# Optimization experiments

Hardware: AMD Instinct MI355X
Metric: run time of the kernel (lower is better)

The kernel has to match this reference:

```python
import jax, jax.numpy as jnp
import numpy as np

ALPHA = 0.2  # LeakyReLU negative slope
MASK_VAL = -9e15


def setup_inputs() -> dict:
    key = jax.random.key(0)
    k1, k2, k3, k4 = jax.random.split(key, 4)
    N, F_IN, F_OUT = 8192, 512, 64
    x = jax.random.normal(k1, (N, F_IN), dtype=jnp.float32)
    adj = jax.random.randint(k2, (N, N), 0, 2, dtype=jnp.int32)
    W = jax.random.normal(k3, (F_IN, F_OUT), dtype=jnp.float32) * (1.414 / np.sqrt(F_IN))
    a = jax.random.normal(k4, (2 * F_OUT, 1), dtype=jnp.float32) * 0.1
    return {"x": x, "adj": adj, "W": W, "a": a}


def reference(x, adj, W, a):
    # h = x @ W : [N, F_OUT]
    h = x @ W
    F_OUT = h.shape[1]
    # additive attention decomposed: score_ij = leaky_relu(a1.h_i + a2.h_j)
    # (mathematically identical to cat([h_i, h_j]) @ a, without the N^2*2F tensor)
    a1 = a[:F_OUT, 0]
    a2 = a[F_OUT:, 0]
    f1 = h @ a1  # [N]
    f2 = h @ a2  # [N]
    e = jax.nn.leaky_relu(f1[:, None] + f2[None, :], negative_slope=ALPHA)  # [N, N]
    e = jnp.where(adj > 0, e, MASK_VAL)
    attention = jax.nn.softmax(e, axis=1)  # dropout p=0.0 / eval mode -> identity
    h_prime = attention @ h  # [N, F_OUT]
    return jax.nn.elu(h_prime)  # concat=True path
```

## Files before the change

kernel.cpp:

```cpp
#include <hip/hip_runtime.h>
#include <stdint.h>

#define NN 8192
#define FIN 512
#define FOUT 64
#define ALPHA 0.2f
#define TJ 512
#define NT (NN / TJ)

typedef float f32x4 __attribute__((ext_vector_type(4)));
typedef int   i32x4 __attribute__((ext_vector_type(4)));
typedef short bf16x8 __attribute__((ext_vector_type(8)));

__device__ __forceinline__ unsigned short f2bf(float f) {
  union { float f; unsigned u; } v; v.f = f;
  unsigned r = (v.u + 0x7fffu + ((v.u >> 16) & 1u)) >> 16;
  return (unsigned short)r;
}

__global__ __launch_bounds__(256) void prep_kernel(
    const float* __restrict__ x, const float* __restrict__ W,
    const float* __restrict__ a, unsigned short* __restrict__ bpack,
    float* __restrict__ f1, float* __restrict__ f2) {
  const int lane = threadIdx.x & 63;
  const int g = blockIdx.x * 4 + (threadIdx.x >> 6);
  const int i0 = g * 8;

  float acc[8];
#pragma unroll
  for (int r = 0; r < 8; ++r) acc[r] = 0.0f;

  for (int k = 0; k < FIN; k += 4) {
    float w0 = W[(k + 0) * FOUT + lane];
    float w1 = W[(k + 1) * FOUT + lane];
    float w2 = W[(k + 2) * FOUT + lane];
    float w3 = W[(k + 3) * FOUT + lane];
#pragma unroll
    for (int r = 0; r < 8; ++r) {
      f32x4 xv = *(const f32x4*)(x + (size_t)(i0 + r) * FIN + k);
      acc[r] = fmaf(xv[0], w0, acc[r]);
      acc[r] = fmaf(xv[1], w1, acc[r]);
      acc[r] = fmaf(xv[2], w2, acc[r]);
      acc[r] = fmaf(xv[3], w3, acc[r]);
    }
  }

  const float a1c = a[lane];
  const float a2c = a[FOUT + lane];
#pragma unroll
  for (int r = 0; r < 8; ++r) {
    float p1 = acc[r] * a1c;
    float p2 = acc[r] * a2c;
#pragma unroll
    for (int off = 32; off >= 1; off >>= 1) {
      p1 += __shfl_xor(p1, off, 64);
      p2 += __shfl_xor(p2, off, 64);
    }
    if (lane == 0) { f1[i0 + r] = p1; f2[i0 + r] = p2; }
  }

  unsigned short hs[8];
#pragma unroll
  for (int r = 0; r < 8; ++r) hs[r] = f2bf(acc[r]);
  const int jb = i0 >> 5;
  const int kg = (i0 >> 3) & 3;
  const int cb = lane >> 4;
  const int rr = lane & 15;
  *(uint4*)(bpack + ((size_t)jb * 2048 + cb * 512 + kg * 128 + rr * 8)) = *(uint4*)hs;
}

__global__ __launch_bounds__(1024, 8) void attn_kernel(
    const int* __restrict__ adj, const unsigned short* __restrict__ bpack,
    const float* __restrict__ f1, const float* __restrict__ f2,
    float* __restrict__ out) {
  __shared__ __align__(16) char lds[16 * 16 * 64 * 4];
  __shared__ float lds_den[16];

  char* pwb0 = lds;
  char* pwb1 = lds + 16384;
  float (*lds_num)[16][64] = (float (*)[16][64])lds;

  const int tid = threadIdx.x;
  const int lane = tid & 63;
  const int wv = tid >> 6;
  const int rg = blockIdx.x;
  const int r15 = lane & 15;
  const int kgrp = lane >> 4;

  const int row_w = rg * 16 + wv;
  const float f1w = f1[row_w];
  const int* adjw = adj + (size_t)row_w * NN;

  int ard = r15 * 1024 + wv * 64 + kgrp * 16;
  ard ^= (r15 & 7) << 4;
  int awr = wv * 1024 + lane * 8;
  awr ^= (wv & 7) << 4;

  f32x4 acc0 = {0.f, 0.f, 0.f, 0.f};
  f32x4 acc1 = acc0, acc2 = acc0, acc3 = acc0;
  float den = 0.0f;

  i32x4 a0 = *(const i32x4*)(adjw + lane * 4);
  i32x4 a1 = *(const i32x4*)(adjw + 256 + lane * 4);

  for (int t = 0; t < NT; ++t) {
    const int j0 = t * TJ;
    f32x4 fA = *(const f32x4*)(f2 + j0 + lane * 4);
    f32x4 fB = *(const f32x4*)(f2 + j0 + 256 + lane * 4);

    unsigned short ws[8];
    float dsum = 0.0f;
#pragma unroll
    for (int e = 0; e < 4; ++e) {
      float s = f1w + fA[e];
      float l = fmaxf(s, ALPHA * s);
      float ev = __expf(l);
      float wv_ = (a0[e] > 0) ? ev : 0.0f;
      dsum += wv_;
      ws[e] = f2bf(wv_);
    }
#pragma unroll
    for (int e = 0; e < 4; ++e) {
      float s = f1w + fB[e];
      float l = fmaxf(s, ALPHA * s);
      float ev = __expf(l);
      float wv_ = (a1[e] > 0) ? ev : 0.0f;
      dsum += wv_;
      ws[4 + e] = f2bf(wv_);
    }
    den += dsum;

    char* pwb = (t & 1) ? pwb1 : pwb0;
    *(uint2*)(pwb + awr) = *(uint2*)&ws[0];
    *(uint2*)(pwb + awr + 512) = *(uint2*)&ws[4];

    __syncthreads();

    const int jn = ((t + 1) & (NT - 1)) * TJ;
    a0 = *(const i32x4*)(adjw + jn + lane * 4);
    a1 = *(const i32x4*)(adjw + jn + 256 + lane * 4);

    bf16x8 afrag = *(bf16x8*)(pwb + ard);
    const unsigned short* bp = bpack + ((size_t)(t * 16 + wv) * 2048 + lane * 8);
    bf16x8 b0 = *(const bf16x8*)(bp);
    bf16x8 b1 = *(const bf16x8*)(bp + 512);
    bf16x8 b2 = *(const bf16x8*)(bp + 1024);
    bf16x8 b3 = *(const bf16x8*)(bp + 1536);

    acc0 = __builtin_amdgcn_mfma_f32_16x16x32_bf16(afrag, b0, acc0, 0, 0, 0);
    acc1 = __builtin_amdgcn_mfma_f32_16x16x32_bf16(afrag, b1, acc1, 0, 0, 0);
    acc2 = __builtin_amdgcn_mfma_f32_16x16x32_bf16(afrag, b2, acc2, 0, 0, 0);
    acc3 = __builtin_amdgcn_mfma_f32_16x16x32_bf16(afrag, b3, acc3, 0, 0, 0);
  }

#pragma unroll
  for (int off = 1; off <= 32; off <<= 1) den += __shfl_xor(den, off, 64);

  __syncthreads();

#pragma unroll
  for (int r = 0; r < 4; ++r) {
    lds_num[wv][kgrp * 4 + r][0 * 16 + r15] = acc0[r];
    lds_num[wv][kgrp * 4 + r][1 * 16 + r15] = acc1[r];
    lds_num[wv][kgrp * 4 + r][2 * 16 + r15] = acc2[r];
    lds_num[wv][kgrp * 4 + r][3 * 16 + r15] = acc3[r];
  }
  if (lane == 0) lds_den[wv] = den;
  __syncthreads();

  {
    const int orow = tid >> 6;
    const int ocol = tid & 63;
    float s = 0.0f;
#pragma unroll
    for (int v = 0; v < 16; ++v) s += lds_num[v][orow][ocol];
    float vv = s / lds_den[orow];
    out[(size_t)(rg * 16 + orow) * FOUT + ocol] = (vv > 0.0f) ? vv : (__expf(vv) - 1.0f);
  }
}

extern "C" void kernel_launch(void* const* d_in, const int* in_sizes, int n_in,
                              void* d_out, int out_size, void* d_ws, size_t ws_size,
                              hipStream_t stream) {
  const float* x = (const float*)d_in[0];
  const int* adj = (const int*)d_in[1];
  const float* W = (const float*)d_in[2];
  const float* a = (const float*)d_in[3];
  float* out = (float*)d_out;

  char* ws = (char*)d_ws;
  unsigned short* bpack = (unsigned short*)ws;
  float* f1 = (float*)(ws + (size_t)FOUT * NN * 2);
  float* f2 = f1 + NN;

  hipLaunchKernelGGL(prep_kernel, dim3(256), dim3(256), 0, stream, x, W, a, bpack, f1, f2);
  hipLaunchKernelGGL(attn_kernel, dim3(512), dim3(1024), 0, stream, adj, bpack, f1, f2, out);
}
```

Before: 127.7 us.

## Pack adjacency into bitmask in a separate pass and prefetch bits in attention

Adds a compact kernel that streams the int32 adjacency matrix once with wide, highly parallel loads and writes a 1-bit-per-entry mask. The attention kernel then reads 8 MB of bits instead of 256 MB of int32 inside its MFMA loop, and software-prefetches the next tile's bits and f2 values. Each lane now handles 8 contiguous columns with a single 16-byte LDS store, and the occupancy hint in the launch bounds is lowered. The extra launch still reads all of adj, so any gain depends on the compaction pass streaming closer to peak bandwidth than the latency-bound attention loop did.

```diff
diff --git a/kernel.cpp b/kernel.cpp
--- a/kernel.cpp
+++ b/kernel.cpp
@@ -16,6 +16,37 @@
   union { float f; unsigned u; } v; v.f = f;
   unsigned r = (v.u + 0x7fffu + ((v.u >> 16) & 1u)) >> 16;
   return (unsigned short)r;
+}
+
+__device__ __forceinline__ unsigned packbits(i32x4 a, i32x4 b) {
+  unsigned r = 0;
+#pragma unroll
+  for (int e = 0; e < 4; ++e) r |= (a[e] > 0 ? 1u : 0u) << e;
+#pragma unroll
+  for (int e = 0; e < 4; ++e) r |= (b[e] > 0 ? 1u : 0u) << (4 + e);
+  return r;
+}
+
+__global__ __launch_bounds__(256) void compact_kernel(
+    const int* __restrict__ adj, unsigned char* __restrict__ bits) {
+  const int lane = threadIdx.x & 63;
+  const int wid = blockIdx.x * 4 + (threadIdx.x >> 6);
+  const int* p0 = adj + (size_t)wid * 2048 + lane * 8;
+
+  i32x4 va0 = *(const i32x4*)(p0);
+  i32x4 vb0 = *(const i32x4*)(p0 + 4);
+  i32x4 va1 = *(const i32x4*)(p0 + 512);
+  i32x4 vb1 = *(const i32x4*)(p0 + 516);
+  i32x4 va2 = *(const i32x4*)(p0 + 1024);
+  i32x4 vb2 = *(const i32x4*)(p0 + 1028);
+  i32x4 va3 = *(const i32x4*)(p0 + 1536);
+  i32x4 vb3 = *(const i32x4*)(p0 + 1540);
+
+  unsigned char* ob = bits + (size_t)wid * 256 + lane;
+  ob[0]   = (unsigned char)packbits(va0, vb0);
+  ob[64]  = (unsigned char)packbits(va1, vb1);
+  ob[128] = (unsigned char)packbits(va2, vb2);
+  ob[192] = (unsigned char)packbits(va3, vb3);
 }
 
 __global__ __launch_bounds__(256) void prep_kernel(
@@ -69,8 +100,8 @@
   *(uint4*)(bpack + ((size_t)jb * 2048 + cb * 512 + kg * 128 + rr * 8)) = *(uint4*)hs;
 }
 
-__global__ __launch_bounds__(1024, 8) void attn_kernel(
-    const int* __restrict__ adj, const unsigned short* __restrict__ bpack,
+__global__ __launch_bounds__(1024, 4) void attn_kernel(
+    const unsigned char* __restrict__ bits, const unsigned short* __restrict__ bpack,
     const float* __restrict__ f1, const float* __restrict__ f2,
     float* __restrict__ out) {
   __shared__ __align__(16) char lds[16 * 16 * 64 * 4];
@@ -89,68 +120,67 @@
 
   const int row_w = rg * 16 + wv;
   const float f1w = f1[row_w];
-  const int* adjw = adj + (size_t)row_w * NN;
+  const unsigned char* bitsrow = bits + (size_t)row_w * (NN / 8);
 
   int ard = r15 * 1024 + wv * 64 + kgrp * 16;
   ard ^= (r15 & 7) << 4;
-  int awr = wv * 1024 + lane * 8;
+  int awr = wv * 1024 + lane * 16;
   awr ^= (wv & 7) << 4;
 
   f32x4 acc0 = {0.f, 0.f, 0.f, 0.f};
   f32x4 acc1 = acc0, acc2 = acc0, acc3 = acc0;
   float den = 0.0f;
 
-  i32x4 a0 = *(const i32x4*)(adjw + lane * 4);
-  i32x4 a1 = *(const i32x4*)(adjw + 256 + lane * 4);
+  unsigned bcur = bitsrow[lane];
+  f32x4 fA = *(const f32x4*)(f2 + lane * 8);
+  f32x4 fB = *(const f32x4*)(f2 + lane * 8 + 4);
 
   for (int t = 0; t < NT; ++t) {
-    const int j0 = t * TJ;
-    f32x4 fA = *(const f32x4*)(f2 + j0 + lane * 4);
-    f32x4 fB = *(const f32x4*)(f2 + j0 + 256 + lane * 4);
-
-    unsigned short ws[8];
-    float dsum = 0.0f;
-#pragma unroll
-    for (int e = 0; e < 4; ++e) {
-      float s = f1w + fA[e];
-      float l = fmaxf(s, ALPHA * s);
-      float ev = __expf(l);
-      float wv_ = (a0[e] > 0) ? ev : 0.0f;
-      dsum += wv_;
-      ws[e] = f2bf(wv_);
-    }
-#pragma unroll
-    for (int e = 0; e < 4; ++e) {
-      float s = f1w + fB[e];
-      float l = fmaxf(s, ALPHA * s);
-      float ev = __expf(l);
-      float wv_ = (a1[e] > 0) ? ev : 0.0f;
-      dsum += wv_;
-      ws[4 + e] = f2bf(wv_);
-    }
-    den += dsum;
-
-    char* pwb = (t & 1) ? pwb1 : pwb0;
-    *(uint2*)(pwb + awr) = *(uint2*)&ws[0];
-    *(uint2*)(pwb + awr + 512) = *(uint2*)&ws[4];
-
-    __syncthreads();
-
-    const int jn = ((t + 1) & (NT - 1)) * TJ;
-    a0 = *(const i32x4*)(adjw + jn + lane * 4);
-    a1 = *(const i32x4*)(adjw + jn + 256 + lane * 4);
-
-    bf16x8 afrag = *(bf16x8*)(pwb + ard);
     const unsigned short* bp = bpack + ((size_t)(t * 16 + wv) * 2048 + lane * 8);
     bf16x8 b0 = *(const bf16x8*)(bp);
     bf16x8 b1 = *(const bf16x8*)(bp + 512);
     bf16x8 b2 = *(const bf16x8*)(bp + 1024);
     bf16x8 b3 = *(const bf16x8*)(bp + 1536);
 
+    const int tn = (t + 1) & (NT - 1);
+    unsigned bnxt = bitsrow[tn * 64 + lane];
+    f32x4 nfA = *(const f32x4*)(f2 + tn * TJ + lane * 8);
+    f32x4 nfB = *(const f32x4*)(f2 + tn * TJ + lane * 8 + 4);
+
+    unsigned short ws8[8];
+    float dsum = 0.0f;
+#pragma unroll
+    for (int e = 0; e < 4; ++e) {
+      float s = f1w + fA[e];
+      float l = fmaxf(s, ALPHA * s);
+      float ev = __expf(l);
+      float w_ = ((bcur >> e) & 1u) ? ev : 0.0f;
+      dsum += w_;
+      ws8[e] = f2bf(w_);
+    }
+#pragma unroll
+    for (int e = 0; e < 4; ++e) {
+      float s = f1w + fB[e];
+      float l = fmaxf(s, ALPHA * s);
+      float ev = __expf(l);
+      float w_ = ((bcur >> (4 + e)) & 1u) ? ev : 0.0f;
+      dsum += w_;
+      ws8[4 + e] = f2bf(w_);
+    }
+    den += dsum;
+
+    char* pwb = (t & 1) ? pwb1 : pwb0;
+    *(uint4*)(pwb + awr) = *(uint4*)ws8;
+
+    __syncthreads();
+
+    bf16x8 afrag = *(bf16x8*)(pwb + ard);
     acc0 = __builtin_amdgcn_mfma_f32_16x16x32_bf16(afrag, b0, acc0, 0, 0, 0);
     acc1 = __builtin_amdgcn_mfma_f32_16x16x32_bf16(afrag, b1, acc1, 0, 0, 0);
     acc2 = __builtin_amdgcn_mfma_f32_16x16x32_bf16(afrag, b2, acc2, 0, 0, 0);
     acc3 = __builtin_amdgcn_mfma_f32_16x16x32_bf16(afrag, b3, acc3, 0, 0, 0);
+
+    bcur = bnxt; fA = nfA; fB = nfB;
   }
 
 #pragma unroll
@@ -192,7 +222,9 @@
   unsigned short* bpack = (unsigned short*)ws;
   float* f1 = (float*)(ws + (size_t)FOUT * NN * 2);
   float* f2 = f1 + NN;
-
+  unsigned char* bits = (unsigned char*)(ws + (2u << 20));
+
+  hipLaunchKernelGGL(compact_kernel, dim3(8192), dim3(256), 0, stream, adj, bits);
   hipLaunchKernelGGL(prep_kernel, dim3(256), dim3(256), 0, stream, x, W, a, bpack, f1, f2);
-  hipLaunchKernelGGL(attn_kernel, dim3(512), dim3(1024), 0, stream, adj, bpack, f1, f2, out);
-}
+  hipLaunchKernelGGL(attn_kernel, dim3(512), dim3(1024), 0, stream, bits, bpack, f1, f2, out);
+}
```

Result: no change. 127.0 us (-0.5%).

## Process 32 rows per block to reuse bpack fragments across two MFMA tiles

Applied to the files above, without the earlier changes.

Each block now handles 32 output rows instead of 16, so every wave computes attention weights for two rows and reuses each loaded h fragment for two MFMA tiles. This halves bpack global reads per output row and halves the grid. The adjacency prefetch is now two tiles deep and the barrier is hand-written asm. The final cross-wave reduction is restructured into two phases with vectorised output stores. In exchange, register pressure and LDS use grow (64 KB per block), which may reduce occupancy.

```diff
diff --git a/kernel.cpp b/kernel.cpp
--- a/kernel.cpp
+++ b/kernel.cpp
@@ -7,8 +7,10 @@
 #define ALPHA 0.2f
 #define TJ 512
 #define NT (NN / TJ)
+#define RB 32
 
 typedef float f32x4 __attribute__((ext_vector_type(4)));
+typedef float f32x2 __attribute__((ext_vector_type(2)));
 typedef int   i32x4 __attribute__((ext_vector_type(4)));
 typedef short bf16x8 __attribute__((ext_vector_type(8)));
 
@@ -69,16 +71,11 @@
   *(uint4*)(bpack + ((size_t)jb * 2048 + cb * 512 + kg * 128 + rr * 8)) = *(uint4*)hs;
 }
 
-__global__ __launch_bounds__(1024, 8) void attn_kernel(
+__global__ __launch_bounds__(1024) void fused_kernel(
     const int* __restrict__ adj, const unsigned short* __restrict__ bpack,
     const float* __restrict__ f1, const float* __restrict__ f2,
     float* __restrict__ out) {
-  __shared__ __align__(16) char lds[16 * 16 * 64 * 4];
-  __shared__ float lds_den[16];
-
-  char* pwb0 = lds;
-  char* pwb1 = lds + 16384;
-  float (*lds_num)[16][64] = (float (*)[16][64])lds;
+  __shared__ __align__(16) char lds[65536 + 128];
 
   const int tid = threadIdx.x;
   const int lane = tid & 63;
@@ -87,95 +84,159 @@
   const int r15 = lane & 15;
   const int kgrp = lane >> 4;
 
-  const int row_w = rg * 16 + wv;
-  const float f1w = f1[row_w];
-  const int* adjw = adj + (size_t)row_w * NN;
-
-  int ard = r15 * 1024 + wv * 64 + kgrp * 16;
-  ard ^= (r15 & 7) << 4;
-  int awr = wv * 1024 + lane * 8;
-  awr ^= (wv & 7) << 4;
-
-  f32x4 acc0 = {0.f, 0.f, 0.f, 0.f};
-  f32x4 acc1 = acc0, acc2 = acc0, acc3 = acc0;
-  float den = 0.0f;
-
-  i32x4 a0 = *(const i32x4*)(adjw + lane * 4);
-  i32x4 a1 = *(const i32x4*)(adjw + 256 + lane * 4);
-
-  for (int t = 0; t < NT; ++t) {
-    const int j0 = t * TJ;
-    f32x4 fA = *(const f32x4*)(f2 + j0 + lane * 4);
-    f32x4 fB = *(const f32x4*)(f2 + j0 + 256 + lane * 4);
-
-    unsigned short ws[8];
-    float dsum = 0.0f;
-#pragma unroll
-    for (int e = 0; e < 4; ++e) {
-      float s = f1w + fA[e];
-      float l = fmaxf(s, ALPHA * s);
-      float ev = __expf(l);
-      float wv_ = (a0[e] > 0) ? ev : 0.0f;
-      dsum += wv_;
-      ws[e] = f2bf(wv_);
-    }
-#pragma unroll
-    for (int e = 0; e < 4; ++e) {
-      float s = f1w + fB[e];
-      float l = fmaxf(s, ALPHA * s);
-      float ev = __expf(l);
-      float wv_ = (a1[e] > 0) ? ev : 0.0f;
-      dsum += wv_;
-      ws[4 + e] = f2bf(wv_);
-    }
-    den += dsum;
-
-    char* pwb = (t & 1) ? pwb1 : pwb0;
-    *(uint2*)(pwb + awr) = *(uint2*)&ws[0];
-    *(uint2*)(pwb + awr + 512) = *(uint2*)&ws[4];
-
-    __syncthreads();
-
-    const int jn = ((t + 1) & (NT - 1)) * TJ;
-    a0 = *(const i32x4*)(adjw + jn + lane * 4);
-    a1 = *(const i32x4*)(adjw + jn + 256 + lane * 4);
-
-    bf16x8 afrag = *(bf16x8*)(pwb + ard);
-    const unsigned short* bp = bpack + ((size_t)(t * 16 + wv) * 2048 + lane * 8);
-    bf16x8 b0 = *(const bf16x8*)(bp);
-    bf16x8 b1 = *(const bf16x8*)(bp + 512);
-    bf16x8 b2 = *(const bf16x8*)(bp + 1024);
-    bf16x8 b3 = *(const bf16x8*)(bp + 1536);
-
-    acc0 = __builtin_amdgcn_mfma_f32_16x16x32_bf16(afrag, b0, acc0, 0, 0, 0);
-    acc1 = __builtin_amdgcn_mfma_f32_16x16x32_bf16(afrag, b1, acc1, 0, 0, 0);
-    acc2 = __builtin_amdgcn_mfma_f32_16x16x32_bf16(afrag, b2, acc2, 0, 0, 0);
-    acc3 = __builtin_amdgcn_mfma_f32_16x16x32_bf16(afrag, b3, acc3, 0, 0, 0);
-  }
-
-#pragma unroll
-  for (int off = 1; off <= 32; off <<= 1) den += __shfl_xor(den, off, 64);
-
-  __syncthreads();
-
-#pragma unroll
-  for (int r = 0; r < 4; ++r) {
-    lds_num[wv][kgrp * 4 + r][0 * 16 + r15] = acc0[r];
-    lds_num[wv][kgrp * 4 + r][1 * 16 + r15] = acc1[r];
-    lds_num[wv][kgrp * 4 + r][2 * 16 + r15] = acc2[r];
-    lds_num[wv][kgrp * 4 + r][3 * 16 + r15] = acc3[r];
-  }
-  if (lane == 0) lds_den[wv] = den;
-  __syncthreads();
+  const int row0 = rg * RB + wv;
+  const int row1 = row0 + 16;
+  const float f1v0 = f1[row0];
+  const float f1v1 = f1[row1];
+  const int* adj0 = adj + (size_t)row0 * NN;
+  const int* adj1 = adj + (size_t)row1 * NN;
+
+  const int aw0 = (wv * 1024 + lane * 16) ^ ((wv & 7) << 4);
+  const int aw1 = ((wv + 16) * 1024 + lane * 16) ^ ((wv & 7) << 4);
+  const int ar0 = (r15 * 1024 + wv * 64 + kgrp * 16) ^ ((r15 & 7) << 4);
+  const int ar1 = ((16 + r15) * 1024 + wv * 64 + kgrp * 16) ^ ((r15 & 7) << 4);
+
+  f32x4 acc00 = {0.f,0.f,0.f,0.f}, acc01 = acc00, acc02 = acc00, acc03 = acc00;
+  f32x4 acc10 = acc00, acc11 = acc00, acc12 = acc00, acc13 = acc00;
+  float den0 = 0.0f, den1 = 0.0f;
+
+  const int jl = lane * 8;
+
+  i32x4 sA0 = *(const i32x4*)(adj0 + jl);
+  i32x4 sA1 = *(const i32x4*)(adj0 + jl + 4);
+  i32x4 sB0 = *(const i32x4*)(adj1 + jl);
+  i32x4 sB1 = *(const i32x4*)(adj1 + jl + 4);
+  f32x4 sFA = *(const f32x4*)(f2 + jl);
+  f32x4 sFB = *(const f32x4*)(f2 + jl + 4);
+  i32x4 tA0 = *(const i32x4*)(adj0 + TJ + jl);
+  i32x4 tA1 = *(const i32x4*)(adj0 + TJ + jl + 4);
+  i32x4 tB0 = *(const i32x4*)(adj1 + TJ + jl);
+  i32x4 tB1 = *(const i32x4*)(adj1 + TJ + jl + 4);
+  f32x4 tFA = *(const f32x4*)(f2 + TJ + jl);
+  f32x4 tFB = *(const f32x4*)(f2 + TJ + jl + 4);
+
+#define FUSED_ITER(T_, CA0, CA1, CB0, CB1, CFA, CFB) do {                           \
+    const int t_ = (T_);                                                            \
+              \
+    const unsigned short* bp = bpack + ((size_t)(t_ * 16 + wv) * 2048) + lane * 8;  \
+    bf16x8 b0 = *(const bf16x8*)(bp);                                               \
+    bf16x8 b1 = *(const bf16x8*)(bp + 512);                                         \
+    bf16x8 b2 = *(const bf16x8*)(bp + 1024);                                        \
+    bf16x8 b3 = *(const bf16x8*)(bp + 1536);                                        \
+                              \
+    unsigned short w0[8], w1[8];                                                    \
+    _Pragma("unroll")                                                               \
+    for (int e = 0; e < 4; ++e) {                                                   \
+      float s0 = f1v0 + CFA[e];                                                     \
+      float v0 = (CA0[e] > 0) ? __expf(fmaxf(s0, ALPHA * s0)) : 0.0f;               \
+      den0 += v0; w0[e] = f2bf(v0);                                                 \
+      float s1 = f1v1 + CFA[e];                                                     \
+      float v1 = (CB0[e] > 0) ? __expf(fmaxf(s1, ALPHA * s1)) : 0.0f;               \
+      den1 += v1; w1[e] = f2bf(v1);                                                 \
+    }                                                                               \
+    _Pragma("unroll")                                                               \
+    for (int e = 0; e < 4; ++e) {                                                   \
+      float s0 = f1v0 + CFB[e];                                                     \
+      float v0 = (CA1[e] > 0) ? __expf(fmaxf(s0, ALPHA * s0)) : 0.0f;               \
+      den0 += v0; w0[4 + e] = f2bf(v0);                                             \
+      float s1 = f1v1 + CFB[e];                                                     \
+      float v1 = (CB1[e] > 0) ? __expf(fmaxf(s1, ALPHA * s1)) : 0.0f;               \
+      den1 += v1; w1[4 + e] = f2bf(v1);                                             \
+    }                                                                               \
+    \
+    {                                                                               \
+      const int j2 = ((t_ + 2) & (NT - 1)) * TJ + jl;                               \
+      CA0 = *(const i32x4*)(adj0 + j2);                                             \
+      CA1 = *(const i32x4*)(adj0 + j2 + 4);                                         \
+      CB0 = *(const i32x4*)(adj1 + j2);                                             \
+      CB1 = *(const i32x4*)(adj1 + j2 + 4);                                         \
+      CFA = *(const f32x4*)(f2 + j2);                                               \
+      CFB = *(const f32x4*)(f2 + j2 + 4);                                           \
+    }                                                                               \
+    char* pwb = lds + (t_ & 1) * 32768;                                             \
+    *(uint4*)(pwb + aw0) = *(uint4*)w0;                                             \
+    *(uint4*)(pwb + aw1) = *(uint4*)w1;                                             \
+                                \
+    asm volatile("s_waitcnt lgkmcnt(0)\n\ts_barrier" ::: "memory");                 \
+    bf16x8 A0 = *(bf16x8*)(pwb + ar0);                                              \
+    bf16x8 A1 = *(bf16x8*)(pwb + ar1);                                              \
+    acc00 = __builtin_amdgcn_mfma_f32_16x16x32_bf16(A0, b0, acc00, 0, 0, 0);        \
+    acc01 = __builtin_amdgcn_mfma_f32_16x16x32_bf16(A0, b1, acc01, 0, 0, 0);        \
+    acc02 = __builtin_amdgcn_mfma_f32_16x16x32_bf16(A0, b2, acc02, 0, 0, 0);        \
+    acc03 = __builtin_amdgcn_mfma_f32_16x16x32_bf16(A0, b3, acc03, 0, 0, 0);        \
+    acc10 = __builtin_amdgcn_mfma_f32_16x16x32_bf16(A1, b0, acc10, 0, 0, 0);        \
+    acc11 = __builtin_amdgcn_mfma_f32_16x16x32_bf16(A1, b1, acc11, 0, 0, 0);        \
+    acc12 = __builtin_amdgcn_mfma_f32_16x16x32_bf16(A1, b2, acc12, 0, 0, 0);        \
+    acc13 = __builtin_amdgcn_mfma_f32_16x16x32_bf16(A1, b3, acc13, 0, 0, 0);        \
+  } while (0)
+
+  for (int tt = 0; tt < NT; tt += 2) {
+    FUSED_ITER(tt,     sA0, sA1, sB0, sB1, sFA, sFB);
+    FUSED_ITER(tt + 1, tA0, tA1, tB0, tB1, tFA, tFB);
+  }
+#undef FUSED_ITER
+
+#pragma unroll
+  for (int off = 1; off <= 32; off <<= 1) {
+    den0 += __shfl_xor(den0, off, 64);
+    den1 += __shfl_xor(den1, off, 64);
+  }
+
+  asm volatile("s_waitcnt lgkmcnt(0)\n\ts_barrier" ::: "memory");
+
+  float* nump = (float*)lds;
+  float* denp = (float*)(lds + 65536);
+  if (lane == 0) { denp[wv] = den0; denp[wv + 16] = den1; }
+
+  if (wv < 8) {
+#pragma unroll
+    for (int r = 0; r < 4; ++r) {
+      const int rl = kgrp * 4 + r;
+      nump[(wv * 32 + rl) * 64 +  0 + r15] = acc00[r];
+      nump[(wv * 32 + rl) * 64 + 16 + r15] = acc01[r];
+      nump[(wv * 32 + rl) * 64 + 32 + r15] = acc02[r];
+      nump[(wv * 32 + rl) * 64 + 48 + r15] = acc03[r];
+      nump[(wv * 32 + 16 + rl) * 64 +  0 + r15] = acc10[r];
+      nump[(wv * 32 + 16 + rl) * 64 + 16 + r15] = acc11[r];
+      nump[(wv * 32 + 16 + rl) * 64 + 32 + r15] = acc12[r];
+      nump[(wv * 32 + 16 + rl) * 64 + 48 + r15] = acc13[r];
+    }
+  }
+  asm volatile("s_waitcnt lgkmcnt(0)\n\ts_barrier" ::: "memory");
+
+  if (wv >= 8) {
+    const int s = wv - 8;
+#pragma unroll
+    for (int r = 0; r < 4; ++r) {
+      const int rl = kgrp * 4 + r;
+      nump[(s * 32 + rl) * 64 +  0 + r15] += acc00[r];
+      nump[(s * 32 + rl) * 64 + 16 + r15] += acc01[r];
+      nump[(s * 32 + rl) * 64 + 32 + r15] += acc02[r];
+      nump[(s * 32 + rl) * 64 + 48 + r15] += acc03[r];
+      nump[(s * 32 + 16 + rl) * 64 +  0 + r15] += acc10[r];
+      nump[(s * 32 + 16 + rl) * 64 + 16 + r15] += acc11[r];
+      nump[(s * 32 + 16 + rl) * 64 + 32 + r15] += acc12[r];
+      nump[(s * 32 + 16 + rl) * 64 + 48 + r15] += acc13[r];
+    }
+  }
+  asm volatile("s_waitcnt lgkmcnt(0)\n\ts_barrier" ::: "memory");
 
   {
-    const int orow = tid >> 6;
-    const int ocol = tid & 63;
-    float s = 0.0f;
-#pragma unroll
-    for (int v = 0; v < 16; ++v) s += lds_num[v][orow][ocol];
-    float vv = s / lds_den[orow];
-    out[(size_t)(rg * 16 + orow) * FOUT + ocol] = (vv > 0.0f) ? vv : (__expf(vv) - 1.0f);
+    const int idx = tid * 2;
+    const int orow = idx >> 6;
+    const int ocol = idx & 63;
+    f32x2 sv = {0.0f, 0.0f};
+#pragma unroll
+    for (int s = 0; s < 8; ++s) {
+      sv[0] += nump[(s * 32 + orow) * 64 + ocol];
+      sv[1] += nump[(s * 32 + orow) * 64 + ocol + 1];
+    }
+    const float d = denp[orow];
+    float v0 = sv[0] / d, v1 = sv[1] / d;
+    v0 = (v0 > 0.0f) ? v0 : (__expf(v0) - 1.0f);
+    v1 = (v1 > 0.0f) ? v1 : (__expf(v1) - 1.0f);
+    f32x2 ov = {v0, v1};
+    *(f32x2*)(out + (size_t)(rg * RB + orow) * FOUT + ocol) = ov;
   }
 }
 
@@ -194,5 +255,6 @@
   float* f2 = f1 + NN;
 
   hipLaunchKernelGGL(prep_kernel, dim3(256), dim3(256), 0, stream, x, W, a, bpack, f1, f2);
-  hipLaunchKernelGGL(attn_kernel, dim3(512), dim3(1024), 0, stream, adj, bpack, f1, f2, out);
-}
+  hipLaunchKernelGGL(fused_kernel, dim3(NN / RB), dim3(1024), 0, stream,
+                     adj, bpack, f1, f2, out);
+}
```

New measurement: 222.7 us. 1.74x slower.
